# Kernel optimization log

Measured on AMD Instinct MI355X. Metric: run time of the kernel, lower is better.

## Reference

```python
import jax, jax.numpy as jnp
import numpy as np

B, T, S, D, H, HD, DFF, NB = 2, 2048, 2048, 768, 12, 64, 3072, 32
HID = H * HD
EPS = 1e-6
NEG = -1e9


def rmsnorm(x, w):
    # T5 RMSNorm: no mean subtraction, no bias
    var = jnp.mean(jnp.square(x), axis=-1, keepdims=True)
    return x * jax.lax.rsqrt(var + EPS) * w


def sdpa(h, kv, m, wq, wk, wv, wo):
    # h: [B,Tq,D], kv: [B,Tk,D], m: additive mask broadcastable to [B,H,Tq,Tk]
    b, tq, _ = h.shape
    tk = kv.shape[1]
    q = (h @ wq).reshape(b, tq, H, HD)
    k = (kv @ wk).reshape(b, tk, H, HD)
    v = (kv @ wv).reshape(b, tk, H, HD)
    scores = jnp.einsum('bthd,bshd->bhts', q, k) + m  # scale=1.0 (T5)
    p = jax.nn.softmax(scores, axis=-1)
    y = jnp.einsum('bhts,bshd->bthd', p, v).reshape(b, tq, HID)
    return y @ wo


def setup_inputs() -> dict:
    key = jax.random.key(0)
    ks = jax.random.split(key, 16)
    x = jax.random.normal(ks[0], (B, T, D), dtype=jnp.float32)
    # causal additive mask for decoder self-attention
    causal = jnp.tril(jnp.ones((T, T), dtype=bool))
    mask = jnp.broadcast_to(jnp.where(causal, 0.0, NEG)[None, None], (B, 1, T, T)).astype(jnp.float32)
    relative_position = jax.random.randint(ks[1], (1, 1, T, T), 0, NB)
    encoder_hidden_states = jax.random.normal(ks[2], (B, S, D), dtype=jnp.float32)
    encoder_attention_mask = jnp.zeros((B, 1, T, S), dtype=jnp.float32)
    sc = 0.02
    p = {
        'sn_w': jnp.ones((D,), jnp.float32),
        'wq': sc * jax.random.normal(ks[3], (D, HID)),
        'wk': sc * jax.random.normal(ks[4], (D, HID)),
        'wv': sc * jax.random.normal(ks[5], (D, HID)),
        'wo': sc * jax.random.normal(ks[6], (HID, D)),
        'rel_emb': sc * jax.random.normal(ks[7], (NB, H)),
        'cn_w': jnp.ones((D,), jnp.float32),
        'cwq': sc * jax.random.normal(ks[8], (D, HID)),
        'cwk': sc * jax.random.normal(ks[9], (D, HID)),
        'cwv': sc * jax.random.normal(ks[10], (D, HID)),
        'cwo': sc * jax.random.normal(ks[11], (HID, D)),
        'pn_w': jnp.ones((D,), jnp.float32),
        'ffn_wi': sc * jax.random.normal(ks[12], (D, DFF)),
        'ffn_wo': sc * jax.random.normal(ks[13], (DFF, D)),
    }
    return dict(x=x, mask=mask, relative_position=relative_position,
                encoder_hidden_states=encoder_hidden_states,
                encoder_attention_mask=encoder_attention_mask, **p)


def reference(x, mask, relative_position, encoder_hidden_states, encoder_attention_mask,
              sn_w, wq, wk, wv, wo, rel_emb, cn_w, cwq, cwk, cwv, cwo, pn_w, ffn_wi, ffn_wo):
    # self-attention with relative-position bias added into additive mask
    h = rmsnorm(x, sn_w)
    # rel_emb[relative_position]: [1,1,T,T,H] -> permute(0,1,4,2,3) -> squeeze(0) -> [1,H,T,T]
    position_bias = jnp.transpose(rel_emb[relative_position], (0, 1, 4, 2, 3))[0]
    self_mask = mask + position_bias
    y = sdpa(h, h, self_mask, wq, wk, wv, wo)
    attn_out = y + x
    # cross-attention (no relative bias -> zeros position bias)
    enc_dec_position_bias = jnp.zeros_like(encoder_attention_mask)
    h2 = rmsnorm(attn_out, cn_w)
    y2 = sdpa(h2, encoder_hidden_states, encoder_attention_mask + enc_dec_position_bias,
              cwq, cwk, cwv, cwo)
    attn_out = y2 + attn_out
    # T5 FFN: relu(x @ wi) @ wo, pre-norm, residual
    hn = rmsnorm(attn_out, pn_w)
    ff = jax.nn.relu(hn @ ffn_wi) @ ffn_wo
    return (attn_out + ff, position_bias, enc_dec_position_bias)
```

## Files before the change

### kernel.cpp

```cpp
#include <hip/hip_runtime.h>
#include <hip/hip_bf16.h>
#include <stdint.h>

#define T5_B   2
#define T5_T   2048
#define T5_S   2048
#define T5_D   768
#define T5_H   12
#define T5_HD  64
#define T5_DFF 3072
#define T5_NB  32
#define NROW   4096

#define LOG2E 1.4426950408889634f

typedef __attribute__((ext_vector_type(8))) short bf16x8;
typedef __attribute__((ext_vector_type(4))) short short4v;
typedef __attribute__((ext_vector_type(4))) float f32x4;
typedef __attribute__((ext_vector_type(16))) float f32x16;

__device__ __forceinline__ unsigned short f2bf(float x) {
  unsigned int u = __float_as_uint(x);
  unsigned int r = (u + 0x7FFFu + ((u >> 16) & 1u)) >> 16;
  return (unsigned short)r;
}

__device__ __forceinline__ float fexp2(float x) {
  float d;
  asm("v_exp_f32 %0, %1" : "=v"(d) : "v"(x));
  return d;
}

__device__ __forceinline__ void load_lds16(const void* g, void* l) {
  __builtin_amdgcn_global_load_lds(
      (__attribute__((address_space(1))) void*)(const_cast<void*>(g)),
      (__attribute__((address_space(3))) void*)(l), 16, 0, 0);
}

__device__ __forceinline__ unsigned cvt_pk_bf16(float lo_, float hi_) {
  unsigned d;
  asm("v_cvt_pk_bf16_f32 %0, %1, %2" : "=v"(d) : "v"(lo_), "v"(hi_));
  return d;
}

__device__ __forceinline__ f32x4 mfma16(short4v a, short4v b, f32x4 c) {
#if __has_builtin(__builtin_amdgcn_mfma_f32_16x16x16bf16_1k)
  return __builtin_amdgcn_mfma_f32_16x16x16bf16_1k(a, b, c, 0, 0, 0);
#else
  asm volatile("v_mfma_f32_16x16x16_bf16 %0, %1, %2, %0" : "+v"(c) : "v"(a), "v"(b));
  return c;
#endif
}

__device__ __forceinline__ int xcd_swz(int f, int nwg) {
  int q8 = nwg >> 3, r8 = nwg & 7, xcd = f & 7, base = f >> 3;
  return (xcd < r8 ? xcd * (q8 + 1) : r8 * (q8 + 1) + (xcd - r8) * q8) + base;
}

template <int TM, int TN, int EPI, int NBUF>
__device__ __forceinline__ void gemm_body(
    int f, int gx, int nwg,
    const unsigned short* __restrict__ A, const unsigned short* __restrict__ Bt,
    void* __restrict__ C, const float* __restrict__ res, int N, int K,
    unsigned short* LDS, unsigned short* vtp = nullptr, int vcol0 = 0, int qe = 0) {
  constexpr bool USE32 = (TM >= 128 && TN >= 128);
  constexpr int WR = (TM >= 128) ? 2 : 1;
  constexpr int WC = 4 / WR;
  constexpr int AM = TM / WR / 16;
  constexpr int AN = TN / WC / 16;
  constexpr int CHA = TM / 8, CHB = TN / 8, CPW = (CHA + CHB) / 4;
  constexpr int BUFSH = (TM + TN) * 64;
  constexpr int DEPTH = NBUF - 1;
  const int tid = threadIdx.x, lane = tid & 63, wv = tid >> 6;
  const int lo = lane & 15, hi = lane >> 4;
  const int l5 = lane >> 5, l31 = lane & 31;
  const int wr = wv / WC, wc = wv % WC;
  const int wg = xcd_swz(f, nwg);
  const int m0 = (wg / gx) * TM, n0 = (wg % gx) * TN;

  f32x4 acc[USE32 ? 1 : AM][USE32 ? 1 : AN];
  f32x16 acc32[USE32 ? 2 : 1][USE32 ? 2 : 1];
  if (USE32) {
#pragma unroll
    for (int i = 0; i < (USE32 ? 2 : 1); ++i)
#pragma unroll
      for (int j = 0; j < (USE32 ? 2 : 1); ++j)
#pragma unroll
        for (int r = 0; r < 16; ++r) acc32[i][j][r] = 0.f;
  } else {
#pragma unroll
    for (int i = 0; i < (USE32 ? 1 : AM); ++i)
#pragma unroll
      for (int j = 0; j < (USE32 ? 1 : AN); ++j) acc[i][j] = f32x4{0.f, 0.f, 0.f, 0.f};
  }

  const int srr  = lane >> 3;
  const int scol = ((lane & 7) ^ srr) * 8;

  auto stage = [&](int k0, int bsel) {
    unsigned short* Ab = LDS + bsel * BUFSH;
    unsigned short* Bb = Ab + TM * 64;
#pragma unroll
    for (int j = 0; j < CPW; ++j) {
      int c = wv * CPW + j;
      if (c < CHA)
        load_lds16(A + (size_t)(m0 + c * 8 + srr) * K + k0 + scol, Ab + c * 512);
      else {
        int c2 = c - CHA;
        load_lds16(Bt + (size_t)(n0 + c2 * 8 + srr) * K + k0 + scol, Bb + c2 * 512);
      }
    }
  };

  const int nIt = K >> 6;
#pragma unroll
  for (int p = 0; p < DEPTH; ++p)
    if (p < nIt) stage(p << 6, p % NBUF);

  for (int it = 0; it < nIt; ++it) {
    const int bsel = it % NBUF;
    if (NBUF == 1) {
      stage(it << 6, 0);
      asm volatile("s_waitcnt vmcnt(0)" ::: "memory");
    } else if (it + DEPTH < nIt) {
      stage((it + DEPTH) << 6, (it + DEPTH) % NBUF);
      asm volatile("s_waitcnt vmcnt(%0)" :: "n"(DEPTH * CPW) : "memory");
    } else if (it + 1 < nIt) {
      asm volatile("s_waitcnt vmcnt(%0)" :: "n"(CPW) : "memory");
    } else {
      asm volatile("s_waitcnt vmcnt(0)" ::: "memory");
    }
    __builtin_amdgcn_s_barrier();
    __builtin_amdgcn_sched_barrier(0);
    const unsigned short* Ab = LDS + bsel * BUFSH;
    const unsigned short* Bb = Ab + TM * 64;
    if (USE32) {
#pragma unroll
      for (int kk = 0; kk < 4; ++kk) {
        bf16x8 af[2], bfr[2];
#pragma unroll
        for (int i = 0; i < 2; ++i) {
          int row = wr * 64 + i * 32 + l31;
          unsigned by = (unsigned)(row * 128) + ((unsigned)(((kk * 2 + l5) ^ (row & 7))) << 4);
          af[i] = *(const bf16x8*)((const char*)Ab + by);
        }
#pragma unroll
        for (int j = 0; j < 2; ++j) {
          int row = wc * 64 + j * 32 + l31;
          unsigned by = (unsigned)(row * 128) + ((unsigned)(((kk * 2 + l5) ^ (row & 7))) << 4);
          bfr[j] = *(const bf16x8*)((const char*)Bb + by);
        }
        __builtin_amdgcn_s_setprio(1);
#pragma unroll
        for (int i = 0; i < 2; ++i)
#pragma unroll
          for (int j = 0; j < 2; ++j)
            acc32[i][j] = __builtin_amdgcn_mfma_f32_32x32x16_bf16(af[i], bfr[j], acc32[i][j], 0, 0, 0);
        __builtin_amdgcn_s_setprio(0);
      }
    } else {
#pragma unroll
      for (int kk = 0; kk < 2; ++kk) {
        bf16x8 af[AM], bfr[AN];
#pragma unroll
        for (int i = 0; i < AM; ++i) {
          int row = wr * (AM * 16) + i * 16 + lo;
          unsigned by = (unsigned)(row * 128) + ((unsigned)(((kk * 4 + hi) ^ (row & 7))) << 4);
          af[i] = *(const bf16x8*)((const char*)Ab + by);
        }
#pragma unroll
        for (int j = 0; j < AN; ++j) {
          int row = wc * (AN * 16) + j * 16 + lo;
          unsigned by = (unsigned)(row * 128) + ((unsigned)(((kk * 4 + hi) ^ (row & 7))) << 4);
          bfr[j] = *(const bf16x8*)((const char*)Bb + by);
        }
        __builtin_amdgcn_s_setprio(1);
#pragma unroll
        for (int i = 0; i < AM; ++i)
#pragma unroll
          for (int j = 0; j < AN; ++j)
            acc[i][j] = __builtin_amdgcn_mfma_f32_16x16x32_bf16(af[i], bfr[j], acc[i][j], 0, 0, 0);
        __builtin_amdgcn_s_setprio(0);
      }
    }
    __builtin_amdgcn_sched_barrier(0);
    __builtin_amdgcn_s_barrier();
  }

  if (USE32) {
#pragma unroll
    for (int i = 0; i < 2; ++i)
#pragma unroll
      for (int j = 0; j < 2; ++j) {
        int colb = n0 + wc * 64 + j * 32 + l31;
#pragma unroll
        for (int g = 0; g < 4; ++g) {
          int rowb = m0 + wr * 64 + i * 32 + g * 8 + 4 * l5;
          if (EPI == 3 && colb >= vcol0) {
            int cc = colb - vcol0, hh = cc >> 6, dd = cc & 63;
            int bb = rowb >> 11, tt = rowb & 2047;
            unsigned long long pk = (unsigned long long)f2bf(acc32[i][j][g * 4 + 0])
                                  | ((unsigned long long)f2bf(acc32[i][j][g * 4 + 1]) << 16)
                                  | ((unsigned long long)f2bf(acc32[i][j][g * 4 + 2]) << 32)
                                  | ((unsigned long long)f2bf(acc32[i][j][g * 4 + 3]) << 48);
            *(unsigned long long*)(vtp + ((size_t)((bb * 12 + hh) * 64 + dd)) * 2048 + tt) = pk;
          } else {
#pragma unroll
            for (int rr = 0; rr < 4; ++rr) {
              float v = acc32[i][j][g * 4 + rr];
              size_t idx = (size_t)(rowb + rr) * N + colb;
              if (EPI == 3) {
                if (colb < qe) v *= LOG2E;
                ((unsigned short*)C)[idx] = f2bf(v);
              } else if (EPI == 0) {
                ((unsigned short*)C)[idx] = f2bf(v);
              } else if (EPI == 1) {
                ((float*)C)[idx] = v + res[idx];
              } else if (EPI == 2) {
                ((unsigned short*)C)[idx] = f2bf(fmaxf(v, 0.0f));
              } else {
                ((unsigned short*)C)[idx] = f2bf(v * LOG2E);
              }
            }
          }
        }
      }
  } else {
#pragma unroll
    for (int mi = 0; mi < (USE32 ? 1 : AM); ++mi)
#pragma unroll
      for (int ni = 0; ni < (USE32 ? 1 : AN); ++ni) {
        int row = m0 + wr * (AM * 16) + mi * 16 + hi * 4;
        int col = n0 + wc * (AN * 16) + ni * 16 + lo;
#pragma unroll
        for (int r = 0; r < 4; ++r) {
          float v = acc[mi][ni][r];
          size_t idx = (size_t)(row + r) * N + col;
          if (EPI == 0 || EPI == 3) {
            ((unsigned short*)C)[idx] = f2bf(v);
          } else if (EPI == 1) {
            ((float*)C)[idx] = v + res[idx];
          } else if (EPI == 2) {
            ((unsigned short*)C)[idx] = f2bf(fmaxf(v, 0.0f));
          } else {
            ((unsigned short*)C)[idx] = f2bf(v * LOG2E);
          }
        }
      }
  }
}

template <int TM, int TN, int EPI, int NBUF>
__global__ __launch_bounds__(256)
void gemm_bt(const unsigned short* __restrict__ A, const unsigned short* __restrict__ Bt,
             void* __restrict__ C, const float* __restrict__ res, int N, int K) {
  __shared__ __align__(16) unsigned short LDS[NBUF * (TM + TN) * 64];
  int f = blockIdx.y * gridDim.x + blockIdx.x;
  gemm_body<TM, TN, EPI, NBUF>(f, gridDim.x, gridDim.x * gridDim.y, A, Bt, C, res, N, K, LDS);
}

struct PrepArgs {
  const float* wsrc[10];
  unsigned short* wdst[10];
  const float* enc; unsigned short* encb;
  const int* rp; unsigned char* rp8;
  const float* x; const float* snw; unsigned short* normb;
};

__global__ __launch_bounds__(256)
void prep_kernel(PrepArgs a) {
  __shared__ __align__(16) float tile[32][33];
  const int bid = blockIdx.x, tid = threadIdx.x;
  if (bid < 9216) {
    int widx, rem, Kd, Nd;
    if (bid < 4608)      { widx = bid / 576; rem = bid % 576;  Kd = 768;  Nd = 768;  }
    else if (bid < 6912) { widx = 8;         rem = bid - 4608; Kd = 768;  Nd = 3072; }
    else                 { widx = 9;         rem = bid - 6912; Kd = 3072; Nd = 768;  }
    const float* W = a.wsrc[widx];
    unsigned short* Wt = a.wdst[widx];
    int nb = Nd / 32;
    int n0 = (rem % nb) * 32, k0 = (rem / nb) * 32;
    int tx = tid & 31, ty = tid >> 5;
#pragma unroll
    for (int i = 0; i < 32; i += 8)
      tile[ty + i][tx] = W[(size_t)(k0 + ty + i) * Nd + n0 + tx];
    __syncthreads();
#pragma unroll
    for (int i = 0; i < 32; i += 8)
      Wt[(size_t)(n0 + ty + i) * Kd + k0 + tx] = f2bf(tile[tx][ty + i]);
  } else if (bid < 12288) {
    int i = (bid - 9216) * 256 + tid;
    float4 v = ((const float4*)a.enc)[i];
    unsigned long long pk = (unsigned long long)f2bf(v.x)
                          | ((unsigned long long)f2bf(v.y) << 16)
                          | ((unsigned long long)f2bf(v.z) << 32)
                          | ((unsigned long long)f2bf(v.w) << 48);
    *(unsigned long long*)(a.encb + (size_t)i * 4) = pk;
  } else if (bid < 13312) {
    int idx = (bid - 12288) * 256 + tid;
    const int4* src = (const int4*)(a.rp + (size_t)idx * 16);
    int4 v0 = src[0], v1 = src[1], v2 = src[2], v3 = src[3];
    uint4 o;
    o.x = (v0.x & 31) | ((v0.y & 31) << 8) | ((v0.z & 31) << 16) | ((v0.w & 31) << 24);
    o.y = (v1.x & 31) | ((v1.y & 31) << 8) | ((v1.z & 31) << 16) | ((v1.w & 31) << 24);
    o.z = (v2.x & 31) | ((v2.y & 31) << 8) | ((v2.z & 31) << 16) | ((v2.w & 31) << 24);
    o.w = (v3.x & 31) | ((v3.y & 31) << 8) | ((v3.z & 31) << 16) | ((v3.w & 31) << 24);
    ((uint4*)a.rp8)[idx] = o;
  } else {
    int row = bid - 13312;
    const float* r = a.x + (size_t)row * 768;
    float x0 = r[tid], x1 = r[tid + 256], x2 = r[tid + 512];
    float s = x0 * x0 + x1 * x1 + x2 * x2;
#pragma unroll
    for (int off = 32; off > 0; off >>= 1) s += __shfl_xor(s, off);
    float* wsm = &tile[0][0];
    int lane = tid & 63, wvv = tid >> 6;
    if (lane == 0) wsm[wvv] = s;
    __syncthreads();
    float tot = wsm[0] + wsm[1] + wsm[2] + wsm[3];
    float rinv = rsqrtf(tot * (1.0f / 768.0f) + 1e-6f);
    unsigned short* o = a.normb + (size_t)row * 768;
    o[tid]       = f2bf(x0 * rinv * a.snw[tid]);
    o[tid + 256] = f2bf(x1 * rinv * a.snw[tid + 256]);
    o[tid + 512] = f2bf(x2 * rinv * a.snw[tid + 512]);
  }
}

__global__ __launch_bounds__(256)
void rmsnorm_kernel(const float* __restrict__ in, const float* __restrict__ w,
                    unsigned short* __restrict__ out) {
  int row = blockIdx.x, tid = threadIdx.x;
  const float* r = in + (size_t)row * 768;
  float x0 = r[tid], x1 = r[tid + 256], x2 = r[tid + 512];
  float s = x0 * x0 + x1 * x1 + x2 * x2;
#pragma unroll
  for (int off = 32; off > 0; off >>= 1) s += __shfl_xor(s, off);
  __shared__ float ws_[4];
  int lane = tid & 63, wv = tid >> 6;
  if (lane == 0) ws_[wv] = s;
  __syncthreads();
  float tot = ws_[0] + ws_[1] + ws_[2] + ws_[3];
  float rinv = rsqrtf(tot * (1.0f / 768.0f) + 1e-6f);
  unsigned short* o = out + (size_t)row * 768;
  o[tid]       = f2bf(x0 * rinv * w[tid]);
  o[tid + 256] = f2bf(x1 * rinv * w[tid + 256]);
  o[tid + 512] = f2bf(x2 * rinv * w[tid + 512]);
}

struct Stage1Args {
  const unsigned short *normb, *wqkvT, *encb, *wckvT;
  unsigned short *qkv, *ckv, *vT1, *vT2;
  const int* rp; const float* rel;
  float *out1, *out2;
};

__global__ __launch_bounds__(256)
void stage1_kernel(Stage1Args a) {
  __shared__ __align__(16) unsigned short LDS[16384];
  const int bid = blockIdx.x, tid = threadIdx.x;
  if (bid < 576) {
    gemm_body<128, 128, 3, 1>(bid, 18, 576, a.normb, a.wqkvT, a.qkv, nullptr, 2304, 768,
                              LDS, a.vT1, 1536, 768);
  } else if (bid < 960) {
    gemm_body<128, 128, 3, 1>(bid - 576, 12, 384, a.encb, a.wckvT, a.ckv, nullptr, 1536, 768,
                              LDS, a.vT2, 768, 0);
  } else {
    const int p = bid - 960;
    float* rl = (float*)LDS;
    for (int i = tid; i < 384; i += 256) rl[i] = a.rel[i];
    __syncthreads();
    int t = p >> 1;
    int s = (p & 1) * 1024 + tid * 4;
    int4 nb = *(const int4*)(a.rp + (size_t)t * 2048 + s);
#pragma unroll
    for (int h = 0; h < 12; ++h) {
      float4 v = make_float4(rl[nb.x * 12 + h], rl[nb.y * 12 + h],
                             rl[nb.z * 12 + h], rl[nb.w * 12 + h]);
      *(float4*)(a.out1 + ((size_t)h * 2048 + t) * 2048 + s) = v;
    }
    size_t zbase = ((size_t)p * 256 + tid) * 8;
    float4 z = make_float4(0.f, 0.f, 0.f, 0.f);
    *(float4*)(a.out2 + zbase)     = z;
    *(float4*)(a.out2 + zbase + 4) = z;
  }
}

template <bool SELF>
__device__ __forceinline__ void attn_qcomp(
    const bf16x8& qf0, const bf16x8& qf1, f32x4* Oc, float& l_,
    const unsigned* nb4, const float* rel_l, int qrow, bool edge, int s0,
    const unsigned short* Kb, const unsigned short* Vb, int lo, int hi) {
  f32x4 S[4];
  __builtin_amdgcn_s_setprio(1);
#pragma unroll
  for (int ct = 0; ct < 4; ++ct) {
    int krow = ct * 16 + lo;
    unsigned by0 = ((unsigned)(krow * 128 + hi * 16))      ^ ((unsigned)(krow & 7) << 4);
    unsigned by1 = ((unsigned)(krow * 128 + 64 + hi * 16)) ^ ((unsigned)(krow & 7) << 4);
    bf16x8 kf0 = *(const bf16x8*)((const char*)Kb + by0);
    bf16x8 kf1 = *(const bf16x8*)((const char*)Kb + by1);
    f32x4 sa = f32x4{0.f, 0.f, 0.f, 0.f};
    sa = __builtin_amdgcn_mfma_f32_16x16x32_bf16(kf0, qf0, sa, 0, 0, 0);
    sa = __builtin_amdgcn_mfma_f32_16x16x32_bf16(kf1, qf1, sa, 0, 0, 0);
    S[ct] = sa;
  }
  __builtin_amdgcn_s_setprio(0);

  if constexpr (SELF) {
#pragma unroll
    for (int ct = 0; ct < 4; ++ct) {
#pragma unroll
      for (int r = 0; r < 4; ++r) {
        int s = s0 + ct * 16 + hi * 4 + r;
        float sc = S[ct][r] + rel_l[(nb4[ct] >> (8 * r)) & 31u];
        if (edge && s > qrow) sc = -1e30f;
        S[ct][r] = sc;
      }
    }
  }

  float rs = 0.f;
#pragma unroll
  for (int ct = 0; ct < 4; ++ct)
#pragma unroll
    for (int r = 0; r < 4; ++r) { float e = fexp2(S[ct][r]); S[ct][r] = e; rs += e; }
  l_ += rs;

  short4v pf[4];
#pragma unroll
  for (int ct = 0; ct < 4; ++ct) {
    union { unsigned u[2]; short4v s; } cv;
    cv.u[0] = cvt_pk_bf16(S[ct][0], S[ct][1]);
    cv.u[1] = cvt_pk_bf16(S[ct][2], S[ct][3]);
    pf[ct] = cv.s;
  }

  __builtin_amdgcn_s_setprio(1);
#pragma unroll
  for (int dt = 0; dt < 4; ++dt) {
    int vrow = dt * 16 + lo;
#pragma unroll
    for (int ct = 0; ct < 4; ++ct) {
      unsigned vb = ((unsigned)(vrow * 128 + ct * 32 + hi * 8)) ^ ((unsigned)(vrow & 7) << 4);
      short4v vf = *(const short4v*)((const char*)Vb + vb);
      Oc[dt] = mfma16(vf, pf[ct], Oc[dt]);
    }
  }
  __builtin_amdgcn_s_setprio(0);
}

__device__ __forceinline__ void attn_store(f32x4* Oc, float l_, unsigned short* yr) {
  l_ += __shfl_xor(l_, 16);
  l_ += __shfl_xor(l_, 32);
  float inv = 1.0f / l_;
#pragma unroll
  for (int dt = 0; dt < 4; ++dt) {
    unsigned long long pk = (unsigned long long)f2bf(Oc[dt][0] * inv)
                          | ((unsigned long long)f2bf(Oc[dt][1] * inv) << 16)
                          | ((unsigned long long)f2bf(Oc[dt][2] * inv) << 32)
                          | ((unsigned long long)f2bf(Oc[dt][3] * inv) << 48);
    *(unsigned long long*)(yr + dt * 16) = pk;
  }
}

__global__ __launch_bounds__(256)
void attn_self_kernel(const unsigned short* __restrict__ qp,
                      const unsigned short* __restrict__ kp,
                      const unsigned short* __restrict__ vT,
                      const unsigned char* __restrict__ rp8,
                      const float* __restrict__ rel_emb,
                      unsigned short* __restrict__ yp) {
  __shared__ __align__(16) unsigned short Kls[2][4096];
  __shared__ __align__(16) unsigned short Vls[2][4096];
  __shared__ float rel_l[32];

  const int tid = threadIdx.x, lane = tid & 63, wv = tid >> 6;
  const int lo = lane & 15, hi = lane >> 4;
  const int wg = xcd_swz(blockIdx.x + 16 * (blockIdx.y + 12 * blockIdx.z), 384);
  const int xq = wg & 15, h = (wg >> 4) % 12, b = (wg >> 4) / 12;
  const int qta = xq, qtb = 31 - xq;
  const int ntiles = qtb + 1;

  if (tid < 32) rel_l[tid] = rel_emb[tid * 12 + h] * LOG2E;

  const int qA = qta * 64 + wv * 16 + lo;
  const int qB = qtb * 64 + wv * 16 + lo;
  const unsigned short* qrA = qp + (size_t)(b * T5_T + qA) * 2304 + h * 64 + hi * 8;
  const unsigned short* qrB = qp + (size_t)(b * T5_T + qB) * 2304 + h * 64 + hi * 8;
  const bf16x8 qa0 = *(const bf16x8*)qrA;
  const bf16x8 qa1 = *(const bf16x8*)(qrA + 32);
  const bf16x8 qb0 = *(const bf16x8*)qrB;
  const bf16x8 qb1 = *(const bf16x8*)(qrB + 32);
  const unsigned char* rpqA = rp8 + (size_t)qA * 2048 + hi * 4;
  const unsigned char* rpqB = rp8 + (size_t)qB * 2048 + hi * 4;

  f32x4 OA[4], OB[4];
  float lA = 0.f, lB = 0.f;
#pragma unroll
  for (int i = 0; i < 4; ++i) { OA[i] = f32x4{0.f, 0.f, 0.f, 0.f}; OB[i] = f32x4{0.f, 0.f, 0.f, 0.f}; }

  const int krr = lane >> 3;
  const int kd0 = ((lane & 7) ^ krr) * 8;

  auto stage = [&](int kt, int bsel) {
    const int s0 = kt * 64;
#pragma unroll
    for (int j = 0; j < 2; ++j) {
      int c = wv * 2 + j;
      int rr = c * 8 + krr;
      load_lds16(kp + (size_t)(b * 2048 + s0 + rr) * 2304 + h * 64 + kd0, &Kls[bsel][c * 512]);
      load_lds16(vT + (size_t)((b * 12 + h) * 64 + rr) * 2048 + s0 + kd0,  &Vls[bsel][c * 512]);
    }
  };

  stage(0, 0);

  for (int kt = 0; kt < ntiles; ++kt) {
    const int bsel = kt & 1;
    const int s0 = kt * 64;
    asm volatile("s_waitcnt vmcnt(0)" ::: "memory");
    __syncthreads();
    unsigned nbA[4], nbB[4];
    if (kt <= qta) {
#pragma unroll
      for (int ct = 0; ct < 4; ++ct) nbA[ct] = *(const unsigned*)(rpqA + s0 + ct * 16);
    }
#pragma unroll
    for (int ct = 0; ct < 4; ++ct) nbB[ct] = *(const unsigned*)(rpqB + s0 + ct * 16);
    if (kt + 1 < ntiles) stage(kt + 1, bsel ^ 1);

    const unsigned short* Kb = &Kls[bsel][0];
    const unsigned short* Vb = &Vls[bsel][0];

    if (kt <= qta)
      attn_qcomp<true>(qa0, qa1, OA, lA, nbA, rel_l, qA, kt == qta, s0, Kb, Vb, lo, hi);
    attn_qcomp<true>(qb0, qb1, OB, lB, nbB, rel_l, qB, kt == qtb, s0, Kb, Vb, lo, hi);
  }

#if !__has_builtin(__builtin_amdgcn_mfma_f32_16x16x16bf16_1k)
  asm volatile("s_nop 7\n\ts_nop 7" ::: );
#endif

  attn_store(OA, lA, yp + (size_t)(b * T5_T + qA) * 768 + h * 64 + hi * 4);
  attn_store(OB, lB, yp + (size_t)(b * T5_T + qB) * 768 + h * 64 + hi * 4);
}

__global__ __launch_bounds__(256)
void attn_cross_kernel(const unsigned short* __restrict__ qp,
                       const unsigned short* __restrict__ kp,
                       const unsigned short* __restrict__ vT,
                       unsigned short* __restrict__ yp) {
  __shared__ __align__(16) unsigned short Kls[2][4096];
  __shared__ __align__(16) unsigned short Vls[2][4096];

  const int tid = threadIdx.x, lane = tid & 63, wv = tid >> 6;
  const int lo = lane & 15, hi = lane >> 4;
  const int wg = xcd_swz(blockIdx.x + 16 * (blockIdx.y + 12 * blockIdx.z), 384);
  const int xq = wg & 15, h = (wg >> 4) % 12, b = (wg >> 4) / 12;

  const int qA = (xq * 2) * 64 + wv * 16 + lo;
  const int qB = (xq * 2 + 1) * 64 + wv * 16 + lo;
  const unsigned short* qrA = qp + (size_t)(b * T5_T + qA) * 768 + h * 64 + hi * 8;
  const unsigned short* qrB = qp + (size_t)(b * T5_T + qB) * 768 + h * 64 + hi * 8;
  const bf16x8 qa0 = *(const bf16x8*)qrA;
  const bf16x8 qa1 = *(const bf16x8*)(qrA + 32);
  const bf16x8 qb0 = *(const bf16x8*)qrB;
  const bf16x8 qb1 = *(const bf16x8*)(qrB + 32);

  f32x4 OA[4], OB[4];
  float lA = 0.f, lB = 0.f;
#pragma unroll
  for (int i = 0; i < 4; ++i) { OA[i] = f32x4{0.f, 0.f, 0.f, 0.f}; OB[i] = f32x4{0.f, 0.f, 0.f, 0.f}; }

  const int krr = lane >> 3;
  const int kd0 = ((lane & 7) ^ krr) * 8;

  auto stage = [&](int kt, int bsel) {
    const int s0 = kt * 64;
#pragma unroll
    for (int j = 0; j < 2; ++j) {
      int c = wv * 2 + j;
      int rr = c * 8 + krr;
      load_lds16(kp + (size_t)(b * 2048 + s0 + rr) * 1536 + h * 64 + kd0, &Kls[bsel][c * 512]);
      load_lds16(vT + (size_t)((b * 12 + h) * 64 + rr) * 2048 + s0 + kd0, &Vls[bsel][c * 512]);
    }
  };

  stage(0, 0);

  for (int kt = 0; kt < 32; ++kt) {
    const int bsel = kt & 1;
    asm volatile("s_waitcnt vmcnt(0)" ::: "memory");
    __syncthreads();
    if (kt + 1 < 32) stage(kt + 1, bsel ^ 1);
    const unsigned short* Kb = &Kls[bsel][0];
    const unsigned short* Vb = &Vls[bsel][0];
    attn_qcomp<false>(qa0, qa1, OA, lA, nullptr, nullptr, 0, false, kt * 64, Kb, Vb, lo, hi);
    attn_qcomp<false>(qb0, qb1, OB, lB, nullptr, nullptr, 0, false, kt * 64, Kb, Vb, lo, hi);
  }

#if !__has_builtin(__builtin_amdgcn_mfma_f32_16x16x16bf16_1k)
  asm volatile("s_nop 7\n\ts_nop 7" ::: );
#endif

  attn_store(OA, lA, yp + (size_t)(b * T5_T + qA) * 768 + h * 64 + hi * 4);
  attn_store(OB, lB, yp + (size_t)(b * T5_T + qB) * 768 + h * 64 + hi * 4);
}

extern "C" void kernel_launch(void* const* d_in, const int* in_sizes, int n_in,
                              void* d_out, int out_size, void* d_ws, size_t ws_size,
                              hipStream_t stream) {
  (void)in_sizes; (void)n_in; (void)out_size; (void)ws_size;
  const float* x    = (const float*)d_in[0];
  const int*   rp   = (const int*)d_in[2];
  const float* enc  = (const float*)d_in[3];
  const float* sn_w = (const float*)d_in[5];
  const float* wq   = (const float*)d_in[6];
  const float* wk   = (const float*)d_in[7];
  const float* wvw  = (const float*)d_in[8];
  const float* wo   = (const float*)d_in[9];
  const float* rel  = (const float*)d_in[10];
  const float* cn_w = (const float*)d_in[11];
  const float* cwq  = (const float*)d_in[12];
  const float* cwk  = (const float*)d_in[13];
  const float* cwv  = (const float*)d_in[14];
  const float* cwo  = (const float*)d_in[15];
  const float* pn_w = (const float*)d_in[16];
  const float* wi   = (const float*)d_in[17];
  const float* wo2  = (const float*)d_in[18];

  float* out0 = (float*)d_out;
  float* out1 = out0 + (size_t)NROW * T5_D;
  float* out2 = out1 + (size_t)T5_H * T5_T * T5_T;

  char* ws = (char*)d_ws;
  size_t off = 0;
  auto alloc = [&](size_t bytes) { char* p = ws + off; off += (bytes + 255) & ~(size_t)255; return p; };
  unsigned short* wqkvT = (unsigned short*)alloc((size_t)2304 * 768 * 2);
  unsigned short* woT   = (unsigned short*)alloc((size_t)768 * 768 * 2);
  unsigned short* wckvT = (unsigned short*)alloc((size_t)1536 * 768 * 2);
  unsigned short* wcqT  = (unsigned short*)alloc((size_t)768 * 768 * 2);
  unsigned short* wcoT  = (unsigned short*)alloc((size_t)768 * 768 * 2);
  unsigned short* wiT   = (unsigned short*)alloc((size_t)3072 * 768 * 2);
  unsigned short* woT2  = (unsigned short*)alloc((size_t)768 * 3072 * 2);
  unsigned short* normb = (unsigned short*)alloc((size_t)NROW * 768 * 2);
  unsigned short* encb  = (unsigned short*)alloc((size_t)NROW * 768 * 2);
  unsigned short* ybuf  = (unsigned short*)alloc((size_t)NROW * 768 * 2);
  unsigned short* cq    = (unsigned short*)alloc((size_t)NROW * 768 * 2);
  float*          attn  = (float*)alloc((size_t)NROW * 768 * 4);
  unsigned char*  rp8p  = (unsigned char*)alloc((size_t)2048 * 2048);
  unsigned short* qkv   = (unsigned short*)alloc((size_t)NROW * 2304 * 2);
  unsigned short* ckv   = (unsigned short*)alloc((size_t)NROW * 1536 * 2);
  unsigned short* vT1   = (unsigned short*)alloc((size_t)24 * 64 * 2048 * 2);
  unsigned short* vT2   = (unsigned short*)alloc((size_t)24 * 64 * 2048 * 2);
  unsigned short* ffh   = (unsigned short*)alloc((size_t)NROW * 3072 * 2);

  dim3 blk(256);

  {
    PrepArgs pa;
    pa.wsrc[0] = wq;  pa.wdst[0] = wqkvT;
    pa.wsrc[1] = wk;  pa.wdst[1] = wqkvT + 768 * 768;
    pa.wsrc[2] = wvw; pa.wdst[2] = wqkvT + 2 * 768 * 768;
    pa.wsrc[3] = wo;  pa.wdst[3] = woT;
    pa.wsrc[4] = cwk; pa.wdst[4] = wckvT;
    pa.wsrc[5] = cwv; pa.wdst[5] = wckvT + 768 * 768;
    pa.wsrc[6] = cwq; pa.wdst[6] = wcqT;
    pa.wsrc[7] = cwo; pa.wdst[7] = wcoT;
    pa.wsrc[8] = wi;  pa.wdst[8] = wiT;
    pa.wsrc[9] = wo2; pa.wdst[9] = woT2;
    pa.enc = enc; pa.encb = encb; pa.rp = rp; pa.rp8 = rp8p;
    pa.x = x; pa.snw = sn_w; pa.normb = normb;
    prep_kernel<<<17408, blk, 0, stream>>>(pa);
  }

  {
    Stage1Args sa;
    sa.normb = normb; sa.wqkvT = wqkvT; sa.encb = encb; sa.wckvT = wckvT;
    sa.qkv = qkv; sa.ckv = ckv; sa.vT1 = vT1; sa.vT2 = vT2;
    sa.rp = rp; sa.rel = rel; sa.out1 = out1; sa.out2 = out2;
    stage1_kernel<<<5056, blk, 0, stream>>>(sa);
  }

  attn_self_kernel<<<dim3(16, 12, 2), blk, 0, stream>>>(qkv, qkv + 768, vT1, rp8p, rel, ybuf);
  gemm_bt<64, 64, 1, 3><<<dim3(12, 64), blk, 0, stream>>>(ybuf, woT, attn, x, 768, 768);

  rmsnorm_kernel<<<NROW, blk, 0, stream>>>(attn, cn_w, normb);
  gemm_bt<64, 64, 4, 3><<<dim3(12, 64), blk, 0, stream>>>(normb, wcqT, cq, nullptr, 768, 768);
  attn_cross_kernel<<<dim3(16, 12, 2), blk, 0, stream>>>(cq, ckv, vT2, ybuf);
  gemm_bt<64, 64, 1, 3><<<dim3(12, 64), blk, 0, stream>>>(ybuf, wcoT, attn, attn, 768, 768);

  rmsnorm_kernel<<<NROW, blk, 0, stream>>>(attn, pn_w, normb);
  gemm_bt<128, 128, 2, 1><<<dim3(24, 32), blk, 0, stream>>>(normb, wiT, ffh, nullptr, 3072, 768);
  gemm_bt<64, 64, 1, 3><<<dim3(12, 64), blk, 0, stream>>>(ffh, woT2, out0, attn, 768, 3072);
}
```

Before: 340.9 us.

## Defer unneeded weight transposes to stage1 and interleave two query tiles in attention

Weight transposes and relative-position packing that are not needed by the first GEMMs move from the prep kernel into extra blocks of the stage1 kernel. This shortens the prep kernel and lets that work overlap with the QKV projection GEMMs. The attention inner step is merged into one function that handles both query tiles together, sharing K/V LDS fragment loads and interleaving their MFMAs. The merged function raises register pressure and makes the causal-skip logic a runtime flag.

```diff
diff --git a/kernel.cpp b/kernel.cpp
--- a/kernel.cpp
+++ b/kernel.cpp
@@ -55,6 +55,22 @@
 __device__ __forceinline__ int xcd_swz(int f, int nwg) {
   int q8 = nwg >> 3, r8 = nwg & 7, xcd = f & 7, base = f >> 3;
   return (xcd < r8 ? xcd * (q8 + 1) : r8 * (q8 + 1) + (xcd - r8) * q8) + base;
+}
+
+__device__ __forceinline__ void wtrans_tile(const float* __restrict__ W,
+                                            unsigned short* __restrict__ Wt,
+                                            int rem, int Kd, int Nd,
+                                            float (*tile)[33], int tid) {
+  int nb = Nd / 32;
+  int n0 = (rem % nb) * 32, k0 = (rem / nb) * 32;
+  int tx = tid & 31, ty = tid >> 5;
+#pragma unroll
+  for (int i = 0; i < 32; i += 8)
+    tile[ty + i][tx] = W[(size_t)(k0 + ty + i) * Nd + n0 + tx];
+  __syncthreads();
+#pragma unroll
+  for (int i = 0; i < 32; i += 8)
+    Wt[(size_t)(n0 + ty + i) * Kd + k0 + tx] = f2bf(tile[tx][ty + i]);
 }
 
 template <int TM, int TN, int EPI, int NBUF>
@@ -260,10 +276,9 @@
 }
 
 struct PrepArgs {
-  const float* wsrc[10];
-  unsigned short* wdst[10];
+  const float* wsrc[5];
+  unsigned short* wdst[5];
   const float* enc; unsigned short* encb;
-  const int* rp; unsigned char* rp8;
   const float* x; const float* snw; unsigned short* normb;
 };
 
@@ -271,43 +286,19 @@
 void prep_kernel(PrepArgs a) {
   __shared__ __align__(16) float tile[32][33];
   const int bid = blockIdx.x, tid = threadIdx.x;
-  if (bid < 9216) {
-    int widx, rem, Kd, Nd;
-    if (bid < 4608)      { widx = bid / 576; rem = bid % 576;  Kd = 768;  Nd = 768;  }
-    else if (bid < 6912) { widx = 8;         rem = bid - 4608; Kd = 768;  Nd = 3072; }
-    else                 { widx = 9;         rem = bid - 6912; Kd = 3072; Nd = 768;  }
-    const float* W = a.wsrc[widx];
-    unsigned short* Wt = a.wdst[widx];
-    int nb = Nd / 32;
-    int n0 = (rem % nb) * 32, k0 = (rem / nb) * 32;
-    int tx = tid & 31, ty = tid >> 5;
-#pragma unroll
-    for (int i = 0; i < 32; i += 8)
-      tile[ty + i][tx] = W[(size_t)(k0 + ty + i) * Nd + n0 + tx];
-    __syncthreads();
-#pragma unroll
-    for (int i = 0; i < 32; i += 8)
-      Wt[(size_t)(n0 + ty + i) * Kd + k0 + tx] = f2bf(tile[tx][ty + i]);
-  } else if (bid < 12288) {
-    int i = (bid - 9216) * 256 + tid;
+  if (bid < 2880) {
+    int widx = bid / 576, rem = bid % 576;
+    wtrans_tile(a.wsrc[widx], a.wdst[widx], rem, 768, 768, tile, tid);
+  } else if (bid < 5952) {
+    int i = (bid - 2880) * 256 + tid;
     float4 v = ((const float4*)a.enc)[i];
     unsigned long long pk = (unsigned long long)f2bf(v.x)
                           | ((unsigned long long)f2bf(v.y) << 16)
                           | ((unsigned long long)f2bf(v.z) << 32)
                           | ((unsigned long long)f2bf(v.w) << 48);
     *(unsigned long long*)(a.encb + (size_t)i * 4) = pk;
-  } else if (bid < 13312) {
-    int idx = (bid - 12288) * 256 + tid;
-    const int4* src = (const int4*)(a.rp + (size_t)idx * 16);
-    int4 v0 = src[0], v1 = src[1], v2 = src[2], v3 = src[3];
-    uint4 o;
-    o.x = (v0.x & 31) | ((v0.y & 31) << 8) | ((v0.z & 31) << 16) | ((v0.w & 31) << 24);
-    o.y = (v1.x & 31) | ((v1.y & 31) << 8) | ((v1.z & 31) << 16) | ((v1.w & 31) << 24);
-    o.z = (v2.x & 31) | ((v2.y & 31) << 8) | ((v2.z & 31) << 16) | ((v2.w & 31) << 24);
-    o.w = (v3.x & 31) | ((v3.y & 31) << 8) | ((v3.z & 31) << 16) | ((v3.w & 31) << 24);
-    ((uint4*)a.rp8)[idx] = o;
   } else {
-    int row = bid - 13312;
+    int row = bid - 5952;
     const float* r = a.x + (size_t)row * 768;
     float x0 = r[tid], x1 = r[tid + 256], x2 = r[tid + 512];
     float s = x0 * x0 + x1 * x1 + x2 * x2;
@@ -352,6 +343,9 @@
   unsigned short *qkv, *ckv, *vT1, *vT2;
   const int* rp; const float* rel;
   float *out1, *out2;
+  const float *wo, *cwq, *cwo, *wi, *wo2;
+  unsigned short *woT, *wcqT, *wcoT, *wiT, *woT2;
+  unsigned char* rp8;
 };
 
 __global__ __launch_bounds__(256)
@@ -364,7 +358,7 @@
   } else if (bid < 960) {
     gemm_body<128, 128, 3, 1>(bid - 576, 12, 384, a.encb, a.wckvT, a.ckv, nullptr, 1536, 768,
                               LDS, a.vT2, 768, 0);
-  } else {
+  } else if (bid < 5056) {
     const int p = bid - 960;
     float* rl = (float*)LDS;
     for (int i = tid; i < 384; i += 256) rl[i] = a.rel[i];
@@ -382,15 +376,37 @@
     float4 z = make_float4(0.f, 0.f, 0.f, 0.f);
     *(float4*)(a.out2 + zbase)     = z;
     *(float4*)(a.out2 + zbase + 4) = z;
+  } else if (bid < 5632) {
+    wtrans_tile(a.wo,  a.woT,  bid - 5056, 768, 768, (float(*)[33])LDS, tid);
+  } else if (bid < 6208) {
+    wtrans_tile(a.cwq, a.wcqT, bid - 5632, 768, 768, (float(*)[33])LDS, tid);
+  } else if (bid < 6784) {
+    wtrans_tile(a.cwo, a.wcoT, bid - 6208, 768, 768, (float(*)[33])LDS, tid);
+  } else if (bid < 9088) {
+    wtrans_tile(a.wi,  a.wiT,  bid - 6784, 768, 3072, (float(*)[33])LDS, tid);
+  } else if (bid < 11392) {
+    wtrans_tile(a.wo2, a.woT2, bid - 9088, 3072, 768, (float(*)[33])LDS, tid);
+  } else {
+    int idx = (bid - 11392) * 256 + tid;
+    const int4* src = (const int4*)(a.rp + (size_t)idx * 16);
+    int4 v0 = src[0], v1 = src[1], v2 = src[2], v3 = src[3];
+    uint4 o;
+    o.x = (v0.x & 31) | ((v0.y & 31) << 8) | ((v0.z & 31) << 16) | ((v0.w & 31) << 24);
+    o.y = (v1.x & 31) | ((v1.y & 31) << 8) | ((v1.z & 31) << 16) | ((v1.w & 31) << 24);
+    o.z = (v2.x & 31) | ((v2.y & 31) << 8) | ((v2.z & 31) << 16) | ((v2.w & 31) << 24);
+    o.w = (v3.x & 31) | ((v3.y & 31) << 8) | ((v3.z & 31) << 16) | ((v3.w & 31) << 24);
+    ((uint4*)a.rp8)[idx] = o;
   }
 }
 
 template <bool SELF>
-__device__ __forceinline__ void attn_qcomp(
-    const bf16x8& qf0, const bf16x8& qf1, f32x4* Oc, float& l_,
-    const unsigned* nb4, const float* rel_l, int qrow, bool edge, int s0,
+__device__ __forceinline__ void attn_qcomp2(
+    const bf16x8& qa0, const bf16x8& qa1, const bf16x8& qb0, const bf16x8& qb1,
+    f32x4* OA, f32x4* OB, float& lA, float& lB,
+    const unsigned* nbA, const unsigned* nbB, const float* rel_l,
+    int qA, int qB, bool doA, bool edgeA, bool edgeB, int s0,
     const unsigned short* Kb, const unsigned short* Vb, int lo, int hi) {
-  f32x4 S[4];
+  f32x4 SA[4], SB[4];
   __builtin_amdgcn_s_setprio(1);
 #pragma unroll
   for (int ct = 0; ct < 4; ++ct) {
@@ -399,52 +415,90 @@
     unsigned by1 = ((unsigned)(krow * 128 + 64 + hi * 16)) ^ ((unsigned)(krow & 7) << 4);
     bf16x8 kf0 = *(const bf16x8*)((const char*)Kb + by0);
     bf16x8 kf1 = *(const bf16x8*)((const char*)Kb + by1);
-    f32x4 sa = f32x4{0.f, 0.f, 0.f, 0.f};
-    sa = __builtin_amdgcn_mfma_f32_16x16x32_bf16(kf0, qf0, sa, 0, 0, 0);
-    sa = __builtin_amdgcn_mfma_f32_16x16x32_bf16(kf1, qf1, sa, 0, 0, 0);
-    S[ct] = sa;
+    if (!SELF || doA) {
+      f32x4 sa = f32x4{0.f, 0.f, 0.f, 0.f};
+      sa = __builtin_amdgcn_mfma_f32_16x16x32_bf16(kf0, qa0, sa, 0, 0, 0);
+      sa = __builtin_amdgcn_mfma_f32_16x16x32_bf16(kf1, qa1, sa, 0, 0, 0);
+      SA[ct] = sa;
+    }
+    f32x4 sb = f32x4{0.f, 0.f, 0.f, 0.f};
+    sb = __builtin_amdgcn_mfma_f32_16x16x32_bf16(kf0, qb0, sb, 0, 0, 0);
+    sb = __builtin_amdgcn_mfma_f32_16x16x32_bf16(kf1, qb1, sb, 0, 0, 0);
+    SB[ct] = sb;
   }
   __builtin_amdgcn_s_setprio(0);
 
   if constexpr (SELF) {
-#pragma unroll
-    for (int ct = 0; ct < 4; ++ct) {
+    if (doA) {
+#pragma unroll
+      for (int ct = 0; ct < 4; ++ct)
+#pragma unroll
+        for (int r = 0; r < 4; ++r) {
+          int s = s0 + ct * 16 + hi * 4 + r;
+          float sc = SA[ct][r] + rel_l[(nbA[ct] >> (8 * r)) & 31u];
+          if (edgeA && s > qA) sc = -1e30f;
+          SA[ct][r] = sc;
+        }
+    }
+#pragma unroll
+    for (int ct = 0; ct < 4; ++ct)
 #pragma unroll
       for (int r = 0; r < 4; ++r) {
         int s = s0 + ct * 16 + hi * 4 + r;
-        float sc = S[ct][r] + rel_l[(nb4[ct] >> (8 * r)) & 31u];
-        if (edge && s > qrow) sc = -1e30f;
-        S[ct][r] = sc;
+        float sc = SB[ct][r] + rel_l[(nbB[ct] >> (8 * r)) & 31u];
+        if (edgeB && s > qB) sc = -1e30f;
+        SB[ct][r] = sc;
       }
-    }
-  }
-
-  float rs = 0.f;
-#pragma unroll
-  for (int ct = 0; ct < 4; ++ct)
-#pragma unroll
-    for (int r = 0; r < 4; ++r) { float e = fexp2(S[ct][r]); S[ct][r] = e; rs += e; }
-  l_ += rs;
-
-  short4v pf[4];
-#pragma unroll
-  for (int ct = 0; ct < 4; ++ct) {
-    union { unsigned u[2]; short4v s; } cv;
-    cv.u[0] = cvt_pk_bf16(S[ct][0], S[ct][1]);
-    cv.u[1] = cvt_pk_bf16(S[ct][2], S[ct][3]);
-    pf[ct] = cv.s;
+  }
+
+  short4v pfA[4], pfB[4];
+  if (!SELF || doA) {
+    float rs = 0.f;
+#pragma unroll
+    for (int ct = 0; ct < 4; ++ct)
+#pragma unroll
+      for (int r = 0; r < 4; ++r) { float e = fexp2(SA[ct][r]); SA[ct][r] = e; rs += e; }
+    lA += rs;
+#pragma unroll
+    for (int ct = 0; ct < 4; ++ct) {
+      union { unsigned u[2]; short4v s; } cv;
+      cv.u[0] = cvt_pk_bf16(SA[ct][0], SA[ct][1]);
+      cv.u[1] = cvt_pk_bf16(SA[ct][2], SA[ct][3]);
+      pfA[ct] = cv.s;
+    }
+  }
+  {
+    float rs = 0.f;
+#pragma unroll
+    for (int ct = 0; ct < 4; ++ct)
+#pragma unroll
+      for (int r = 0; r < 4; ++r) { float e = fexp2(SB[ct][r]); SB[ct][r] = e; rs += e; }
+    lB += rs;
+#pragma unroll
+    for (int ct = 0; ct < 4; ++ct) {
+      union { unsigned u[2]; short4v s; } cv;
+      cv.u[0] = cvt_pk_bf16(SB[ct][0], SB[ct][1]);
+      cv.u[1] = cvt_pk_bf16(SB[ct][2], SB[ct][3]);
+      pfB[ct] = cv.s;
+    }
   }
 
   __builtin_amdgcn_s_setprio(1);
 #pragma unroll
   for (int dt = 0; dt < 4; ++dt) {
     int vrow = dt * 16 + lo;
+    short4v vf[4];
 #pragma unroll
     for (int ct = 0; ct < 4; ++ct) {
       unsigned vb = ((unsigned)(vrow * 128 + ct * 32 + hi * 8)) ^ ((unsigned)(vrow & 7) << 4);
-      short4v vf = *(const short4v*)((const char*)Vb + vb);
-      Oc[dt] = mfma16(vf, pf[ct], Oc[dt]);
-    }
+      vf[ct] = *(const short4v*)((const char*)Vb + vb);
+    }
+    if (!SELF || doA) {
+#pragma unroll
+      for (int ct = 0; ct < 4; ++ct) OA[dt] = mfma16(vf[ct], pfA[ct], OA[dt]);
+    }
+#pragma unroll
+    for (int ct = 0; ct < 4; ++ct) OB[dt] = mfma16(vf[ct], pfB[ct], OB[dt]);
   }
   __builtin_amdgcn_s_setprio(0);
 }
@@ -520,8 +574,9 @@
     const int s0 = kt * 64;
     asm volatile("s_waitcnt vmcnt(0)" ::: "memory");
     __syncthreads();
+    const bool doA = (kt <= qta);
     unsigned nbA[4], nbB[4];
-    if (kt <= qta) {
+    if (doA) {
 #pragma unroll
       for (int ct = 0; ct < 4; ++ct) nbA[ct] = *(const unsigned*)(rpqA + s0 + ct * 16);
     }
@@ -529,12 +584,9 @@
     for (int ct = 0; ct < 4; ++ct) nbB[ct] = *(const unsigned*)(rpqB + s0 + ct * 16);
     if (kt + 1 < ntiles) stage(kt + 1, bsel ^ 1);
 
-    const unsigned short* Kb = &Kls[bsel][0];
-    const unsigned short* Vb = &Vls[bsel][0];
-
-    if (kt <= qta)
-      attn_qcomp<true>(qa0, qa1, OA, lA, nbA, rel_l, qA, kt == qta, s0, Kb, Vb, lo, hi);
-    attn_qcomp<true>(qb0, qb1, OB, lB, nbB, rel_l, qB, kt == qtb, s0, Kb, Vb, lo, hi);
+    attn_qcomp2<true>(qa0, qa1, qb0, qb1, OA, OB, lA, lB, nbA, nbB, rel_l,
+                      qA, qB, doA, kt == qta, kt == qtb, s0,
+                      &Kls[bsel][0], &Vls[bsel][0], lo, hi);
   }
 
 #if !__has_builtin(__builtin_amdgcn_mfma_f32_16x16x16bf16_1k)
@@ -593,10 +645,9 @@
     asm volatile("s_waitcnt vmcnt(0)" ::: "memory");
     __syncthreads();
     if (kt + 1 < 32) stage(kt + 1, bsel ^ 1);
-    const unsigned short* Kb = &Kls[bsel][0];
-    const unsigned short* Vb = &Vls[bsel][0];
-    attn_qcomp<false>(qa0, qa1, OA, lA, nullptr, nullptr, 0, false, kt * 64, Kb, Vb, lo, hi);
-    attn_qcomp<false>(qb0, qb1, OB, lB, nullptr, nullptr, 0, false, kt * 64, Kb, Vb, lo, hi);
+    attn_qcomp2<false>(qa0, qa1, qb0, qb1, OA, OB, lA, lB, nullptr, nullptr, nullptr,
+                       0, 0, true, false, false, kt * 64,
+                       &Kls[bsel][0], &Vls[bsel][0], lo, hi);
   }
 
 #if !__has_builtin(__builtin_amdgcn_mfma_f32_16x16x16bf16_1k)
@@ -662,16 +713,11 @@
     pa.wsrc[0] = wq;  pa.wdst[0] = wqkvT;
     pa.wsrc[1] = wk;  pa.wdst[1] = wqkvT + 768 * 768;
     pa.wsrc[2] = wvw; pa.wdst[2] = wqkvT + 2 * 768 * 768;
-    pa.wsrc[3] = wo;  pa.wdst[3] = woT;
-    pa.wsrc[4] = cwk; pa.wdst[4] = wckvT;
-    pa.wsrc[5] = cwv; pa.wdst[5] = wckvT + 768 * 768;
-    pa.wsrc[6] = cwq; pa.wdst[6] = wcqT;
-    pa.wsrc[7] = cwo; pa.wdst[7] = wcoT;
-    pa.wsrc[8] = wi;  pa.wdst[8] = wiT;
-    pa.wsrc[9] = wo2; pa.wdst[9] = woT2;
-    pa.enc = enc; pa.encb = encb; pa.rp = rp; pa.rp8 = rp8p;
+    pa.wsrc[3] = cwk; pa.wdst[3] = wckvT;
+    pa.wsrc[4] = cwv; pa.wdst[4] = wckvT + 768 * 768;
+    pa.enc = enc; pa.encb = encb;
     pa.x = x; pa.snw = sn_w; pa.normb = normb;
-    prep_kernel<<<17408, blk, 0, stream>>>(pa);
+    prep_kernel<<<10048, blk, 0, stream>>>(pa);
   }
 
   {
@@ -679,7 +725,10 @@
     sa.normb = normb; sa.wqkvT = wqkvT; sa.encb = encb; sa.wckvT = wckvT;
     sa.qkv = qkv; sa.ckv = ckv; sa.vT1 = vT1; sa.vT2 = vT2;
     sa.rp = rp; sa.rel = rel; sa.out1 = out1; sa.out2 = out2;
-    stage1_kernel<<<5056, blk, 0, stream>>>(sa);
+    sa.wo = wo; sa.cwq = cwq; sa.cwo = cwo; sa.wi = wi; sa.wo2 = wo2;
+    sa.woT = woT; sa.wcqT = wcqT; sa.wcoT = wcoT; sa.wiT = wiT; sa.woT2 = woT2;
+    sa.rp8 = rp8p;
+    stage1_kernel<<<12416, blk, 0, stream>>>(sa);
   }
 
   attn_self_kernel<<<dim3(16, 12, 2), blk, 0, stream>>>(qkv, qkv + 768, vT1, rp8p, rel, ybuf);
```

After: 332.9 us. -2.3%, faster.
